# Kernel tuning notes

Measured on AMD Instinct MI355X. Metric: run time of the kernel, lower is better.

## Reference

```python
import jax, jax.numpy as jnp
import numpy as np

IN_CHANNELS = 2  # density + 1 value channel
OUT_CHANNELS = 64
INIT_LENGTH_SCALE = 0.03125


def setup_inputs() -> dict:
    key = jax.random.key(0)
    ks = jax.random.split(key, 5)
    B, N_IN, N_OUT = 8, 1024, 4096
    # locations in roughly [-2, 2]
    x = jax.random.uniform(ks[0], (B, N_IN, 2), jnp.float32, -2.0, 2.0)
    y = jax.random.normal(ks[1], (B, N_IN, 1), jnp.float32)
    t = jax.random.uniform(ks[2], (B, N_OUT, 2), jnp.float32, -2.0, 2.0)
    # learned params
    sigma = jnp.full((IN_CHANNELS,), np.log(INIT_LENGTH_SCALE), jnp.float32)
    W = jax.random.normal(ks[3], (OUT_CHANNELS, IN_CHANNELS), jnp.float32) / jnp.sqrt(IN_CHANNELS)
    b = jnp.zeros((OUT_CHANNELS,), jnp.float32)
    return {"x": x, "y": y, "t": t, "sigma": sigma, "W": W, "b": b}


def reference(x, y, t, sigma, W, b):
    # pairwise squared distances over 2D coords: (B, n_in, n_out)
    dists = ((x[:, :, None, 0] - t[:, None, :, 0]) ** 2
             + (x[:, :, None, 1] - t[:, None, :, 1]) ** 2)
    scales = jnp.exp(sigma)  # (C,) with C = in_channels = 2
    # RBF weights per channel: (B, n_in, n_out, C)
    wt = jnp.exp(-0.5 * dists[..., None] / scales ** 2)
    B, n_in, _ = x.shape
    density = jnp.ones((B, n_in, 1), x.dtype)
    dens_y = jnp.concatenate([density, y], axis=2)  # (B, n_in, C)
    # weighted sum over context points: (B, n_out, C)
    y_out = jnp.einsum('bnc,bnmc->bmc', dens_y, wt)
    dens, conv = y_out[..., :1], y_out[..., 1:]
    feat = jnp.concatenate([dens, conv / (dens + 1e-8)], axis=-1)  # (B, n_out, C)
    # pointwise linear to out_channels
    return jnp.einsum('bmc,oc->bmo', feat, W) + b
```

## Files before the change

kernel.cpp:

```cpp
#include <hip/hip_runtime.h>


#define OUTC 64
#define MB   64
#define NW   16

__global__ __launch_bounds__(1024, 8) void convdeepset_kernel(
    const float* __restrict__ x,
    const float* __restrict__ y,
    const float* __restrict__ t,
    const float* __restrict__ sigma,
    const float* __restrict__ W,
    const float* __restrict__ bias,
    float* __restrict__ out)
{
    __shared__ float4 pk[1024];
    __shared__ float  dens_part[NW*MB];
    __shared__ float  conv_part[NW*MB];
    __shared__ float  sums[2*MB];
    __shared__ float  dens_tot[MB];
    __shared__ float  ratio[MB];

    const int tid = threadIdx.x;
    const int b   = blockIdx.x >> 6;
    const int m0  = (blockIdx.x & 63) * MB;

    const float log2e = 1.44269504088896340736f;
    const float k0 = -0.5f * __expf(-2.0f * sigma[0]) * log2e;
    const float k1 = -0.5f * __expf(-2.0f * sigma[1]) * log2e;
    const float s0 = sqrtf(-k0);
    const float r  = k1 / k0;

    {
        const float2 xv = ((const float2*)(x + (size_t)b * 2048))[tid];
        const float  yv = y[(size_t)b * 1024 + tid];
        const float sx = xv.x * s0, sy = xv.y * s0;
        pk[tid] = make_float4(sx + sx, sy + sy,
                              -fmaf(sx, sx, sy * sy), yv);
    }

    const int wave = tid >> 6;
    const int lane = tid & 63;
    const float2 tv = ((const float2*)(t + ((size_t)b * 4096 + m0) * 2))[lane];
    const float u  = tv.x * s0;
    const float v  = tv.y * s0;
    const float cm = -fmaf(u, u, v * v);

    __syncthreads();

    float dacc = 0.f, cacc = 0.f;
    const int ibeg = wave * 64;

    if (r == 1.0f) {
        #pragma unroll 4
        for (int i = ibeg; i < ibeg + 64; ++i) {
            const float4 p = pk[i];
            float arg = fmaf(p.x, u, fmaf(p.y, v, p.z + cm));
            float e   = __builtin_amdgcn_exp2f(arg);
            dacc += e;
            cacc = fmaf(p.w, e, cacc);
        }
    } else {
        #pragma unroll 2
        for (int i = ibeg; i < ibeg + 64; ++i) {
            const float4 p = pk[i];
            float arg = fmaf(p.x, u, fmaf(p.y, v, p.z + cm));
            dacc += __builtin_amdgcn_exp2f(arg);
            cacc = fmaf(p.w, __builtin_amdgcn_exp2f(arg * r), cacc);
        }
    }

    dens_part[wave * MB + lane] = dacc;
    conv_part[wave * MB + lane] = cacc;
    __syncthreads();

    if (tid < 2 * MB) {
        const int m = tid & (MB - 1);
        const float* src = (tid < MB) ? dens_part : conv_part;
        float s = 0.f;
        #pragma unroll
        for (int w = 0; w < NW; ++w) s += src[w * MB + m];
        sums[tid] = s;
    }
    __syncthreads();
    if (tid < MB) {
        float dt = sums[tid];
        dens_tot[tid] = dt;
        ratio[tid]    = sums[MB + tid] / (dt + 1e-8f);
    }
    __syncthreads();

    const int o = tid & 63;
    const int g = tid >> 6;
    const float w0 = W[o * 2 + 0];
    const float w1 = W[o * 2 + 1];
    const float bo = bias[o];
    float* outb = out + ((size_t)b * 4096 + m0) * OUTC;
    #pragma unroll
    for (int i = 0; i < 4; ++i) {
        int mm = g * 4 + i;
        outb[mm * OUTC + o] = fmaf(dens_tot[mm], w0, fmaf(ratio[mm], w1, bo));
    }
}

extern "C" void kernel_launch(void* const* d_in, const int* in_sizes, int n_in,
                              void* d_out, int out_size, void* d_ws, size_t ws_size,
                              hipStream_t stream) {
    const float* x     = (const float*)d_in[0];
    const float* y     = (const float*)d_in[1];
    const float* t     = (const float*)d_in[2];
    const float* sigma = (const float*)d_in[3];
    const float* W     = (const float*)d_in[4];
    const float* bias  = (const float*)d_in[5];
    float* out = (float*)d_out;

    convdeepset_kernel<<<dim3(512), dim3(1024), 0, stream>>>(
        x, y, t, sigma, W, bias, out);
}
```

Baseline: 72.57 us.

## Process two target points per thread using packed f32x2 math

```diff
diff --git a/kernel.cpp b/kernel.cpp
--- a/kernel.cpp
+++ b/kernel.cpp
@@ -2,10 +2,12 @@
 
 
 #define OUTC 64
-#define MB   64
+#define MB   128
 #define NW   16
 
-__global__ __launch_bounds__(1024, 8) void convdeepset_kernel(
+typedef __attribute__((ext_vector_type(2))) float f32x2;
+
+__global__ __launch_bounds__(1024, 4) void convdeepset_kernel(
     const float* __restrict__ x,
     const float* __restrict__ y,
     const float* __restrict__ t,
@@ -22,8 +24,8 @@
     __shared__ float  ratio[MB];
 
     const int tid = threadIdx.x;
-    const int b   = blockIdx.x >> 6;
-    const int m0  = (blockIdx.x & 63) * MB;
+    const int b   = blockIdx.x >> 5;
+    const int m0  = (blockIdx.x & 31) * MB;
 
     const float log2e = 1.44269504088896340736f;
     const float k0 = -0.5f * __expf(-2.0f * sigma[0]) * log2e;
@@ -41,37 +43,54 @@
 
     const int wave = tid >> 6;
     const int lane = tid & 63;
-    const float2 tv = ((const float2*)(t + ((size_t)b * 4096 + m0) * 2))[lane];
-    const float u  = tv.x * s0;
-    const float v  = tv.y * s0;
-    const float cm = -fmaf(u, u, v * v);
+    const float2* tg = (const float2*)(t + ((size_t)b * 4096 + m0) * 2);
+    const float2 ta = tg[lane];
+    const float2 tb = tg[64 + lane];
+    f32x2 u2, v2, cm2;
+    u2.x = ta.x * s0;  u2.y = tb.x * s0;
+    v2.x = ta.y * s0;  v2.y = tb.y * s0;
+    cm2.x = -fmaf(u2.x, u2.x, v2.x * v2.x);
+    cm2.y = -fmaf(u2.y, u2.y, v2.y * v2.y);
 
     __syncthreads();
 
-    float dacc = 0.f, cacc = 0.f;
+    f32x2 dacc = {0.f, 0.f}, cacc = {0.f, 0.f};
     const int ibeg = wave * 64;
 
     if (r == 1.0f) {
         #pragma unroll 4
         for (int i = ibeg; i < ibeg + 64; ++i) {
             const float4 p = pk[i];
-            float arg = fmaf(p.x, u, fmaf(p.y, v, p.z + cm));
-            float e   = __builtin_amdgcn_exp2f(arg);
+            f32x2 arg = cm2 + p.z;
+            arg = __builtin_elementwise_fma((f32x2)p.x, u2, arg);
+            arg = __builtin_elementwise_fma((f32x2)p.y, v2, arg);
+            f32x2 e;
+            e.x = __builtin_amdgcn_exp2f(arg.x);
+            e.y = __builtin_amdgcn_exp2f(arg.y);
             dacc += e;
-            cacc = fmaf(p.w, e, cacc);
+            cacc = __builtin_elementwise_fma((f32x2)p.w, e, cacc);
         }
     } else {
         #pragma unroll 2
         for (int i = ibeg; i < ibeg + 64; ++i) {
             const float4 p = pk[i];
-            float arg = fmaf(p.x, u, fmaf(p.y, v, p.z + cm));
-            dacc += __builtin_amdgcn_exp2f(arg);
-            cacc = fmaf(p.w, __builtin_amdgcn_exp2f(arg * r), cacc);
+            f32x2 arg = cm2 + p.z;
+            arg = __builtin_elementwise_fma((f32x2)p.x, u2, arg);
+            arg = __builtin_elementwise_fma((f32x2)p.y, v2, arg);
+            f32x2 e, er;
+            e.x  = __builtin_amdgcn_exp2f(arg.x);
+            e.y  = __builtin_amdgcn_exp2f(arg.y);
+            er.x = __builtin_amdgcn_exp2f(arg.x * r);
+            er.y = __builtin_amdgcn_exp2f(arg.y * r);
+            dacc += e;
+            cacc = __builtin_elementwise_fma((f32x2)p.w, er, cacc);
         }
     }
 
-    dens_part[wave * MB + lane] = dacc;
-    conv_part[wave * MB + lane] = cacc;
+    dens_part[wave * MB + lane]      = dacc.x;
+    dens_part[wave * MB + 64 + lane] = dacc.y;
+    conv_part[wave * MB + lane]      = cacc.x;
+    conv_part[wave * MB + 64 + lane] = cacc.y;
     __syncthreads();
 
     if (tid < 2 * MB) {
@@ -97,8 +116,8 @@
     const float bo = bias[o];
     float* outb = out + ((size_t)b * 4096 + m0) * OUTC;
     #pragma unroll
-    for (int i = 0; i < 4; ++i) {
-        int mm = g * 4 + i;
+    for (int i = 0; i < 8; ++i) {
+        int mm = g * 8 + i;
         outb[mm * OUTC + o] = fmaf(dens_tot[mm], w0, fmaf(ratio[mm], w1, bo));
     }
 }
@@ -114,6 +133,6 @@
     const float* bias  = (const float*)d_in[5];
     float* out = (float*)d_out;
 
-    convdeepset_kernel<<<dim3(512), dim3(1024), 0, stream>>>(
+    convdeepset_kernel<<<dim3(256), dim3(1024), 0, stream>>>(
         x, y, t, sigma, W, bias, out);
 }
```

Result: no change. 72.50 us (-0.1%).
